# Kernel tuning notes

Hardware: AMD Instinct MI355X
Metric: run time of the kernel (lower is better)

Reference implementation:

```python
import jax, jax.numpy as jnp
import numpy as np

N_NODES = 50000
N_EDGES = 600000
FEAT = 128
N_RBF = 20
CUTOFF = 5.0


def setup_inputs() -> dict:
    key = jax.random.key(0)
    ks = jax.random.split(key, 8)
    s_j = jax.random.normal(ks[0], (N_NODES, FEAT), dtype=jnp.float32)
    # distances in (0.1, cutoff) to avoid div-by-zero in the sinc basis
    dist = jax.random.uniform(ks[1], (N_EDGES,), dtype=jnp.float32) * (CUTOFF - 0.1) + 0.1
    nbrs = jax.random.randint(ks[2], (N_EDGES, 2), 0, N_NODES, dtype=jnp.int64)
    scale = 1.0 / np.sqrt(FEAT)
    W1 = jax.random.normal(ks[3], (FEAT, FEAT), dtype=jnp.float32) * scale
    b1 = jnp.zeros((FEAT,), dtype=jnp.float32)
    W2 = jax.random.normal(ks[4], (FEAT, 3 * FEAT), dtype=jnp.float32) * scale
    b2 = jnp.zeros((3 * FEAT,), dtype=jnp.float32)
    Wd = jax.random.normal(ks[5], (N_RBF, 3 * FEAT), dtype=jnp.float32) / np.sqrt(N_RBF)
    bd = jnp.zeros((3 * FEAT,), dtype=jnp.float32)
    return {"s_j": s_j, "dist": dist, "nbrs": nbrs,
            "W1": W1, "b1": b1, "W2": W2, "b2": b2, "Wd": Wd, "bd": bd}


def _radial_basis(dist):
    # sin(n*pi*d/cutoff)/d for n = 1..N_RBF  -> [E, N_RBF]
    n = jnp.arange(1, N_RBF + 1, dtype=dist.dtype)
    d = dist[:, None]
    return jnp.sin(n * jnp.pi * d / CUTOFF) / d


def reference(s_j, dist, nbrs, W1, b1, W2, b2, Wd, bd):
    # gather neighbor features: [E, FEAT]
    sj = s_j[nbrs[:, 1]]
    # 2-layer MLP with swish: [E, 3*FEAT]
    h = sj @ W1 + b1
    h = h * jax.nn.sigmoid(h)  # swish
    phi = h @ W2 + b2
    # distance embedding: RBF -> dense: [E, 3*FEAT]
    w_s = _radial_basis(dist) @ Wd + bd
    out = phi * w_s
    return out.reshape(out.shape[0], -1, 3)  # [E, FEAT, 3]
```

## Files before the change

kernel.cpp:

```cpp
#include <hip/hip_runtime.h>
#include <math.h>

#define FEAT 128
#define OUTF 384
#define NRBF 20
#define EILP 8

typedef float f32x2 __attribute__((ext_vector_type(2)));
typedef float f32x4 __attribute__((ext_vector_type(4)));
typedef _Float16 f16x4 __attribute__((ext_vector_type(4)));
typedef _Float16 f16x8 __attribute__((ext_vector_type(8)));

__device__ __forceinline__ int nbrs_is_i64(const int* nb) {
    int nz = 0;
#pragma unroll
    for (int i = 1; i < 64; i += 2) nz |= nb[i];
    return nz == 0;
}

__global__ __launch_bounds__(256) void prep_w_kernel(
    const float* __restrict__ W1, const float* __restrict__ W2,
    _Float16* __restrict__ w1f, _Float16* __restrict__ w2f)
{
    int idx = blockIdx.x * 256 + threadIdx.x;
    if (idx < 8 * 4 * 64) {
        int ct = idx >> 8, ks = (idx >> 6) & 3, lane = idx & 63;
        int lcol = lane & 15, lgrp = lane >> 4;
        _Float16* dst = w1f + (size_t)idx * 8;
        const float* src = W1 + (size_t)(ks * 32 + lgrp * 8) * FEAT + ct * 16 + lcol;
#pragma unroll
        for (int j = 0; j < 8; j++) dst[j] = (_Float16)src[(size_t)j * FEAT];
    } else {
        int i2 = idx - 2048;
        if (i2 < 24 * 4 * 64) {
            int ct = i2 >> 8, ks = (i2 >> 6) & 3, lane = i2 & 63;
            int lcol = lane & 15, lgrp = lane >> 4;
            _Float16* dst = w2f + (size_t)i2 * 8;
            const float* src = W2 + (size_t)(ks * 32 + lgrp * 8) * OUTF + ct * 16 + lcol;
#pragma unroll
            for (int j = 0; j < 8; j++) dst[j] = (_Float16)src[(size_t)j * OUTF];
        }
    }
}

__global__ __launch_bounds__(256) void phi_mfma_kernel(
    const float* __restrict__ s_j,
    const _Float16* __restrict__ w1f, const float* __restrict__ b1,
    const _Float16* __restrict__ w2f, const float* __restrict__ b2,
    _Float16* __restrict__ PHI, int M)
{
    __shared__ __align__(16) float s32[64][136];
    __shared__ __align__(16) _Float16 h16[4][16][144];
    const int t = threadIdx.x;
    const int base = blockIdx.x * 64;

    for (int idx = t; idx < 64 * 32; idx += 256) {
        int row = idx >> 5, c4 = (idx & 31) * 4;
        float4 v = {0.f, 0.f, 0.f, 0.f};
        if (base + row < M) v = *(const float4*)(s_j + (size_t)(base + row) * FEAT + c4);
        *(float4*)&s32[row][c4] = v;
    }
    __syncthreads();

    const int w = t >> 6, lane = t & 63;
    const int lcol = lane & 15;
    const int lgrp = lane >> 4;
    const int r0 = w * 16;

    f16x8 a1[4];
#pragma unroll
    for (int ks = 0; ks < 4; ks++) {
        const float* p = &s32[r0 + lcol][ks * 32 + lgrp * 8];
        float4 u = *(const float4*)p;
        float4 v = *(const float4*)(p + 4);
        a1[ks] = (f16x8){(_Float16)u.x, (_Float16)u.y, (_Float16)u.z, (_Float16)u.w,
                         (_Float16)v.x, (_Float16)v.y, (_Float16)v.z, (_Float16)v.w};
    }

#pragma unroll
    for (int ct = 0; ct < 8; ct++) {
        float bb = b1[ct * 16 + lcol];
        f32x4 acc = {bb, bb, bb, bb};
#pragma unroll
        for (int ks = 0; ks < 4; ks++) {
            f16x8 b = *(const f16x8*)(w1f + ((size_t)(ct * 4 + ks) * 64 + lane) * 8);
            acc = __builtin_amdgcn_mfma_f32_16x16x32_f16(a1[ks], b, acc, 0, 0, 0);
        }
#pragma unroll
        for (int r = 0; r < 4; r++) {
            float h = acc[r];
            h = h * __frcp_rn(1.f + __expf(-h));
            h16[w][lgrp * 4 + r][ct * 16 + lcol] = (_Float16)h;
        }
    }

    f16x8 a2[4];
#pragma unroll
    for (int ks = 0; ks < 4; ks++)
        a2[ks] = *(const f16x8*)&h16[w][lcol][ks * 32 + lgrp * 8];

    for (int ch = 0; ch < 3; ch++) {
#pragma unroll
        for (int c8 = 0; c8 < 8; c8++) {
            int ct = ch * 8 + c8;
            float bb = b2[ct * 16 + lcol];
            f32x4 acc = {bb, bb, bb, bb};
#pragma unroll
            for (int ks = 0; ks < 4; ks++) {
                f16x8 b = *(const f16x8*)(w2f + ((size_t)(ct * 4 + ks) * 64 + lane) * 8);
                acc = __builtin_amdgcn_mfma_f32_16x16x32_f16(a2[ks], b, acc, 0, 0, 0);
            }
#pragma unroll
            for (int r = 0; r < 4; r++)
                h16[w][lgrp * 4 + r][c8 * 16 + lcol] = (_Float16)acc[r];
        }
#pragma unroll
        for (int i = 0; i < 4; i++) {
            int flat = i * 64 + lane;
            int row = flat >> 4, cc = (flat & 15) * 8;
            int grow = base + r0 + row;
            if (grow < M) {
                f16x8 v = *(const f16x8*)&h16[w][row][cc];
                *(f16x8*)(PHI + (size_t)grow * OUTF + ch * 128 + cc) = v;
            }
        }
    }
}

template <bool GATHER, bool HALF_OUT>
__global__ __launch_bounds__(256) void phi_kernel(
    const float* __restrict__ s_j, const int* __restrict__ nbrs,
    const float* __restrict__ W1, const float* __restrict__ b1,
    const float* __restrict__ W2, const float* __restrict__ b2,
    void* __restrict__ dst_v, int M)
{
    __shared__ __align__(16) float st[FEAT][66];
    const int t = threadIdx.x;
    const int base = blockIdx.x * 64;

    int i64f = 0;
    if (GATHER) i64f = nbrs_is_i64(nbrs);

    for (int idx = t; idx < 64 * FEAT; idx += 256) {
        int n = idx >> 7, k = idx & 127;
        int row = base + n;
        float v = 0.f;
        if (row < M) {
            int src = GATHER ? (i64f ? nbrs[4 * (size_t)row + 2] : nbrs[2 * (size_t)row + 1])
                             : row;
            v = s_j[(size_t)src * FEAT + k];
        }
        st[k][n] = v;
    }
    __syncthreads();

    const int cg = t & 31, rg = t >> 5;
    const int c0 = cg * 4, r0 = rg * 8;

    float acc[8][4];
    {
        float4 b = *(const float4*)(b1 + c0);
#pragma unroll
        for (int i = 0; i < 8; i++) { acc[i][0] = b.x; acc[i][1] = b.y; acc[i][2] = b.z; acc[i][3] = b.w; }
#pragma unroll 4
        for (int k = 0; k < FEAT; k++) {
            float4 w = *(const float4*)(W1 + (size_t)k * FEAT + c0);
            float2 sa = *(const float2*)(&st[k][r0]);
            float2 sb = *(const float2*)(&st[k][r0 + 2]);
            float2 sc = *(const float2*)(&st[k][r0 + 4]);
            float2 sd = *(const float2*)(&st[k][r0 + 6]);
            float sv[8] = {sa.x, sa.y, sb.x, sb.y, sc.x, sc.y, sd.x, sd.y};
#pragma unroll
            for (int i = 0; i < 8; i++) {
                acc[i][0] += sv[i] * w.x; acc[i][1] += sv[i] * w.y;
                acc[i][2] += sv[i] * w.z; acc[i][3] += sv[i] * w.w;
            }
        }
    }
    __syncthreads();
#pragma unroll
    for (int i = 0; i < 8; i++)
#pragma unroll
        for (int j = 0; j < 4; j++) {
            float h = acc[i][j];
            h = h * __frcp_rn(1.f + __expf(-h));
            st[c0 + j][r0 + i] = h;
        }
    __syncthreads();

    for (int ch = 0; ch < 3; ch++) {
        const int oc = ch * 128 + c0;
        float4 b = *(const float4*)(b2 + oc);
#pragma unroll
        for (int i = 0; i < 8; i++) { acc[i][0] = b.x; acc[i][1] = b.y; acc[i][2] = b.z; acc[i][3] = b.w; }
#pragma unroll 4
        for (int k = 0; k < FEAT; k++) {
            float4 w = *(const float4*)(W2 + (size_t)k * OUTF + oc);
            float2 ha = *(const float2*)(&st[k][r0]);
            float2 hb = *(const float2*)(&st[k][r0 + 2]);
            float2 hc = *(const float2*)(&st[k][r0 + 4]);
            float2 hd = *(const float2*)(&st[k][r0 + 6]);
            float hv[8] = {ha.x, ha.y, hb.x, hb.y, hc.x, hc.y, hd.x, hd.y};
#pragma unroll
            for (int i = 0; i < 8; i++) {
                acc[i][0] += hv[i] * w.x; acc[i][1] += hv[i] * w.y;
                acc[i][2] += hv[i] * w.z; acc[i][3] += hv[i] * w.w;
            }
        }
#pragma unroll
        for (int i = 0; i < 8; i++) {
            int row = base + r0 + i;
            if (row < M) {
                if (HALF_OUT) {
                    f16x4 o = {(_Float16)acc[i][0], (_Float16)acc[i][1],
                               (_Float16)acc[i][2], (_Float16)acc[i][3]};
                    *(f16x4*)((_Float16*)dst_v + (size_t)row * OUTF + oc) = o;
                } else {
                    float4 o = {acc[i][0], acc[i][1], acc[i][2], acc[i][3]};
                    *(float4*)((float*)dst_v + (size_t)row * OUTF + oc) = o;
                }
            }
        }
    }
}

template <bool FP16PHI>
__global__ __launch_bounds__(384)
__attribute__((amdgpu_waves_per_eu(3, 3)))
void edge_kernel(
    const float* __restrict__ dist, const int* __restrict__ nbrs,
    const void* phi_v, const float* __restrict__ Wd,
    const float* __restrict__ bd, float* out,
    int E, int gather)
{
    __shared__ __align__(16) f32x4 wdl[NRBF][96];
    const int t = threadIdx.x;
    for (int idx = t; idx < NRBF * 96; idx += 384) {
        int n = idx / 96, qq = idx % 96;
        wdl[n][qq] = *(const f32x4*)(Wd + (size_t)n * OUTF + qq * 4);
    }
    __syncthreads();

    const int g = t / 96;
    const int q = t % 96;
    const int c0 = q * 4;

    f32x4 bdr = *(const f32x4*)(bd + c0);

    int i64f = gather ? nbrs_is_i64(nbrs) : 0;
    const float kx = (float)(M_PI / 5.0);
    const int stride = gridDim.x * (4 * EILP);

    for (int e = (blockIdx.x * 4 + g) * EILP; e < E; e += stride) {
        float d[EILP];
        int r[EILP];
#pragma unroll
        for (int j = 0; j < EILP; j++) {
            int ej = e + j; if (ej >= E) ej = E - 1;
            d[j] = dist[ej];
            r[j] = gather ? (i64f ? nbrs[4 * (size_t)ej + 2] : nbrs[2 * (size_t)ej + 1]) : ej;
        }
        f32x4 p[EILP];
#pragma unroll
        for (int j = 0; j < EILP; j++) {
            if (FP16PHI) {
                const _Float16* ph = (const _Float16*)phi_v;
                f16x4 h = *(const f16x4*)(ph + (size_t)r[j] * OUTF + c0);
                p[j] = (f32x4){(float)h.x, (float)h.y, (float)h.z, (float)h.w};
            } else {
                const float* pf = (const float*)phi_v;
                p[j] = *(const f32x4*)(pf + (size_t)r[j] * OUTF + c0);
            }
        }

        float t2[EILP], sp[EILP], sc[EILP];
#pragma unroll
        for (int j = 0; j < EILP; j++) {
            float s, c;
            __sincosf(d[j] * kx, &s, &c);
            sc[j] = s;
            t2[j] = 2.f * c;
            sp[j] = 0.f;
        }
        f32x4 a[EILP];
#pragma unroll
        for (int j = 0; j < EILP; j++) a[j] = (f32x4){0.f, 0.f, 0.f, 0.f};
#pragma unroll
        for (int n = 0; n < NRBF; n++) {
            f32x4 w = wdl[n][q];
#pragma unroll
            for (int j = 0; j < EILP; j++) {
                a[j] += sc[j] * w;
                float nx = t2[j] * sc[j] - sp[j]; sp[j] = sc[j]; sc[j] = nx;
            }
        }
#pragma unroll
        for (int j = 0; j < EILP; j++) {
            if (e + j < E) {
                f32x4 o = p[j] * (a[j] * __frcp_rn(d[j]) + bdr);
                __builtin_nontemporal_store(o, (f32x4*)(out + (size_t)(e + j) * OUTF + c0));
            }
        }
    }
}

extern "C" void kernel_launch(void* const* d_in, const int* in_sizes, int n_in,
                              void* d_out, int out_size, void* d_ws, size_t ws_size,
                              hipStream_t stream)
{
    const float* s_j  = (const float*)d_in[0];
    const float* dist = (const float*)d_in[1];
    const int*   nbrs = (const int*)d_in[2];
    const float* W1   = (const float*)d_in[3];
    const float* b1   = (const float*)d_in[4];
    const float* W2   = (const float*)d_in[5];
    const float* b2   = (const float*)d_in[6];
    const float* Wd   = (const float*)d_in[7];
    const float* bd   = (const float*)d_in[8];
    float* out = (float*)d_out;

    const int N = in_sizes[0] / FEAT;
    const int E = in_sizes[1];
    if (E <= 0) return;

    const size_t phi_bytes = (size_t)N * OUTF * sizeof(_Float16);
    const size_t w1_off = phi_bytes;
    const size_t w2_off = w1_off + (size_t)8 * 4 * 64 * 8 * 2;
    const size_t need   = w2_off + (size_t)24 * 4 * 64 * 8 * 2;

    int egrid = (E + 4 * EILP - 1) / (4 * EILP);
    if (egrid > 2048) egrid = 2048;

    if (ws_size >= need) {
        _Float16* PHI = (_Float16*)d_ws;
        _Float16* w1f = (_Float16*)((char*)d_ws + w1_off);
        _Float16* w2f = (_Float16*)((char*)d_ws + w2_off);
        prep_w_kernel<<<32, 256, 0, stream>>>(W1, W2, w1f, w2f);
        phi_mfma_kernel<<<(N + 63) / 64, 256, 0, stream>>>(s_j, w1f, b1, w2f, b2, PHI, N);
        edge_kernel<true><<<egrid, 384, 0, stream>>>(dist, nbrs, PHI, Wd, bd, out, E, 1);
    } else {
        dim3 gA((E + 63) / 64);
        phi_kernel<true, false><<<gA, 256, 0, stream>>>(s_j, nbrs, W1, b1, W2, b2, d_out, E);
        edge_kernel<false><<<egrid, 384, 0, stream>>>(dist, nbrs, d_out, Wd, bd, out, E, 0);
    }
}
```

Measured before the change: 277.4 us.

## Compute distance embedding with fp16 MFMA in a new edge kernel

Adds an edge kernel that builds each edge's 20-term sinc radial basis in registers and multiplies it by a pre-packed fp16 Wd using a 16x16x32 MFMA, then scales by the gathered fp16 phi row. The prep kernel now also packs Wd into the MFMA operand layout. This removes the per-edge scalar FMA loop over RBF terms and the LDS staging of Wd. The trade-offs are fp16 rounding of the basis and weights, and output stores that are split into 64-byte pieces per edge row instead of contiguous full-row writes.

```diff
diff --git a/kernel.cpp b/kernel.cpp
--- a/kernel.cpp
+++ b/kernel.cpp
@@ -4,9 +4,7 @@
 #define FEAT 128
 #define OUTF 384
 #define NRBF 20
-#define EILP 8
-
-typedef float f32x2 __attribute__((ext_vector_type(2)));
+
 typedef float f32x4 __attribute__((ext_vector_type(4)));
 typedef _Float16 f16x4 __attribute__((ext_vector_type(4)));
 typedef _Float16 f16x8 __attribute__((ext_vector_type(8)));
@@ -20,7 +18,9 @@
 
 __global__ __launch_bounds__(256) void prep_w_kernel(
     const float* __restrict__ W1, const float* __restrict__ W2,
-    _Float16* __restrict__ w1f, _Float16* __restrict__ w2f)
+    const float* __restrict__ Wd,
+    _Float16* __restrict__ w1f, _Float16* __restrict__ w2f,
+    _Float16* __restrict__ wdf)
 {
     int idx = blockIdx.x * 256 + threadIdx.x;
     if (idx < 8 * 4 * 64) {
@@ -30,15 +30,26 @@
         const float* src = W1 + (size_t)(ks * 32 + lgrp * 8) * FEAT + ct * 16 + lcol;
 #pragma unroll
         for (int j = 0; j < 8; j++) dst[j] = (_Float16)src[(size_t)j * FEAT];
+    } else if (idx < 8192) {
+        int i2 = idx - 2048;
+        int ct = i2 >> 8, ks = (i2 >> 6) & 3, lane = i2 & 63;
+        int lcol = lane & 15, lgrp = lane >> 4;
+        _Float16* dst = w2f + (size_t)i2 * 8;
+        const float* src = W2 + (size_t)(ks * 32 + lgrp * 8) * OUTF + ct * 16 + lcol;
+#pragma unroll
+        for (int j = 0; j < 8; j++) dst[j] = (_Float16)src[(size_t)j * OUTF];
     } else {
-        int i2 = idx - 2048;
-        if (i2 < 24 * 4 * 64) {
-            int ct = i2 >> 8, ks = (i2 >> 6) & 3, lane = i2 & 63;
+        int i3 = idx - 8192;
+        if (i3 < 24 * 64) {
+            int ct = i3 >> 6, lane = i3 & 63;
             int lcol = lane & 15, lgrp = lane >> 4;
-            _Float16* dst = w2f + (size_t)i2 * 8;
-            const float* src = W2 + (size_t)(ks * 32 + lgrp * 8) * OUTF + ct * 16 + lcol;
-#pragma unroll
-            for (int j = 0; j < 8; j++) dst[j] = (_Float16)src[(size_t)j * OUTF];
+            _Float16* dst = wdf + (size_t)i3 * 8;
+#pragma unroll
+            for (int j = 0; j < 8; j++) {
+                int k = lgrp * 8 + j;
+                dst[j] = (k < NRBF) ? (_Float16)Wd[(size_t)k * OUTF + ct * 16 + lcol]
+                                    : (_Float16)0.f;
+            }
         }
     }
 }
@@ -127,12 +138,74 @@
     }
 }
 
-template <bool GATHER, bool HALF_OUT>
+__global__ __launch_bounds__(256) void edge_mfma_kernel(
+    const float* __restrict__ dist, const int* __restrict__ nbrs,
+    const _Float16* __restrict__ PHI, const _Float16* __restrict__ wdf,
+    const float* __restrict__ bd, float* __restrict__ out, int E)
+{
+    const int t = threadIdx.x;
+    const int w = t >> 6, lane = t & 63;
+    const int lcol = lane & 15, lgrp = lane >> 4;
+
+    const int i64f = nbrs_is_i64(nbrs);
+    const int e = blockIdx.x * 64 + w * 16 + lcol;
+    const int ec = (e < E) ? e : (E - 1);
+    const bool ok = (e < E);
+
+    const float d = dist[ec];
+    const int ridx = i64f ? nbrs[4 * (size_t)ec + 2] : nbrs[2 * (size_t)ec + 1];
+
+    const float kx = (float)(M_PI / 5.0);
+    float v[NRBF];
+    {
+        float s, c;
+        __sincosf(d * kx, &s, &c);
+        float rd = __frcp_rn(d);
+        float t2 = 2.f * c;
+        float sp = 0.f, sc = s;
+        v[0] = s * rd;
+#pragma unroll
+        for (int n = 1; n < NRBF; n++) {
+            float nx = t2 * sc - sp; sp = sc; sc = nx;
+            v[n] = sc * rd;
+        }
+    }
+    f16x8 bf;
+    if (lgrp == 0)
+        bf = (f16x8){(_Float16)v[0], (_Float16)v[1], (_Float16)v[2], (_Float16)v[3],
+                     (_Float16)v[4], (_Float16)v[5], (_Float16)v[6], (_Float16)v[7]};
+    else if (lgrp == 1)
+        bf = (f16x8){(_Float16)v[8], (_Float16)v[9], (_Float16)v[10], (_Float16)v[11],
+                     (_Float16)v[12], (_Float16)v[13], (_Float16)v[14], (_Float16)v[15]};
+    else if (lgrp == 2)
+        bf = (f16x8){(_Float16)v[16], (_Float16)v[17], (_Float16)v[18], (_Float16)v[19],
+                     (_Float16)0.f, (_Float16)0.f, (_Float16)0.f, (_Float16)0.f};
+    else
+        bf = (f16x8){(_Float16)0.f, (_Float16)0.f, (_Float16)0.f, (_Float16)0.f,
+                     (_Float16)0.f, (_Float16)0.f, (_Float16)0.f, (_Float16)0.f};
+
+    const _Float16* phirow = PHI + (size_t)ridx * OUTF;
+    float* orow = out + (size_t)ec * OUTF;
+
+#pragma unroll 4
+    for (int ct = 0; ct < 24; ct++) {
+        const int c0 = ct * 16 + lgrp * 4;
+        f16x8 af = *(const f16x8*)(wdf + ((size_t)(ct * 64 + lane)) * 8);
+        f32x4 acc = *(const f32x4*)(bd + c0);
+        acc = __builtin_amdgcn_mfma_f32_16x16x32_f16(af, bf, acc, 0, 0, 0);
+        f16x4 p = *(const f16x4*)(phirow + c0);
+        f32x4 o = {(float)p.x * acc[0], (float)p.y * acc[1],
+                   (float)p.z * acc[2], (float)p.w * acc[3]};
+        if (ok) __builtin_nontemporal_store(o, (f32x4*)(orow + c0));
+    }
+}
+
+template <bool GATHER>
 __global__ __launch_bounds__(256) void phi_kernel(
     const float* __restrict__ s_j, const int* __restrict__ nbrs,
     const float* __restrict__ W1, const float* __restrict__ b1,
     const float* __restrict__ W2, const float* __restrict__ b2,
-    void* __restrict__ dst_v, int M)
+    float* __restrict__ dst, int M)
 {
     __shared__ __align__(16) float st[FEAT][66];
     const int t = threadIdx.x;
@@ -211,27 +284,19 @@
         for (int i = 0; i < 8; i++) {
             int row = base + r0 + i;
             if (row < M) {
-                if (HALF_OUT) {
-                    f16x4 o = {(_Float16)acc[i][0], (_Float16)acc[i][1],
-                               (_Float16)acc[i][2], (_Float16)acc[i][3]};
-                    *(f16x4*)((_Float16*)dst_v + (size_t)row * OUTF + oc) = o;
-                } else {
-                    float4 o = {acc[i][0], acc[i][1], acc[i][2], acc[i][3]};
-                    *(float4*)((float*)dst_v + (size_t)row * OUTF + oc) = o;
-                }
-            }
-        }
-    }
-}
-
-template <bool FP16PHI>
+                float4 o = {acc[i][0], acc[i][1], acc[i][2], acc[i][3]};
+                *(float4*)(dst + (size_t)row * OUTF + oc) = o;
+            }
+        }
+    }
+}
+
 __global__ __launch_bounds__(384)
 __attribute__((amdgpu_waves_per_eu(3, 3)))
 void edge_kernel(
     const float* __restrict__ dist, const int* __restrict__ nbrs,
-    const void* phi_v, const float* __restrict__ Wd,
-    const float* __restrict__ bd, float* out,
-    int E, int gather)
+    const float* phi, const float* __restrict__ Wd,
+    const float* __restrict__ bd, float* out, int E)
 {
     __shared__ __align__(16) f32x4 wdl[NRBF][96];
     const int t = threadIdx.x;
@@ -244,58 +309,45 @@
     const int g = t / 96;
     const int q = t % 96;
     const int c0 = q * 4;
-
     f32x4 bdr = *(const f32x4*)(bd + c0);
 
-    int i64f = gather ? nbrs_is_i64(nbrs) : 0;
     const float kx = (float)(M_PI / 5.0);
-    const int stride = gridDim.x * (4 * EILP);
-
-    for (int e = (blockIdx.x * 4 + g) * EILP; e < E; e += stride) {
-        float d[EILP];
-        int r[EILP];
-#pragma unroll
-        for (int j = 0; j < EILP; j++) {
+    const int stride = gridDim.x * 32;
+
+    for (int e = (blockIdx.x * 4 + g) * 8; e < E; e += stride) {
+        float d[8]; int r[8];
+#pragma unroll
+        for (int j = 0; j < 8; j++) {
             int ej = e + j; if (ej >= E) ej = E - 1;
             d[j] = dist[ej];
-            r[j] = gather ? (i64f ? nbrs[4 * (size_t)ej + 2] : nbrs[2 * (size_t)ej + 1]) : ej;
-        }
-        f32x4 p[EILP];
-#pragma unroll
-        for (int j = 0; j < EILP; j++) {
-            if (FP16PHI) {
-                const _Float16* ph = (const _Float16*)phi_v;
-                f16x4 h = *(const f16x4*)(ph + (size_t)r[j] * OUTF + c0);
-                p[j] = (f32x4){(float)h.x, (float)h.y, (float)h.z, (float)h.w};
-            } else {
-                const float* pf = (const float*)phi_v;
-                p[j] = *(const f32x4*)(pf + (size_t)r[j] * OUTF + c0);
-            }
-        }
-
-        float t2[EILP], sp[EILP], sc[EILP];
-#pragma unroll
-        for (int j = 0; j < EILP; j++) {
+            r[j] = ej;
+        }
+        f32x4 p[8];
+#pragma unroll
+        for (int j = 0; j < 8; j++)
+            p[j] = *(const f32x4*)(phi + (size_t)r[j] * OUTF + c0);
+
+        float t2[8], sp[8], sc[8];
+#pragma unroll
+        for (int j = 0; j < 8; j++) {
             float s, c;
             __sincosf(d[j] * kx, &s, &c);
-            sc[j] = s;
-            t2[j] = 2.f * c;
-            sp[j] = 0.f;
-        }
-        f32x4 a[EILP];
-#pragma unroll
-        for (int j = 0; j < EILP; j++) a[j] = (f32x4){0.f, 0.f, 0.f, 0.f};
+            sc[j] = s; t2[j] = 2.f * c; sp[j] = 0.f;
+        }
+        f32x4 a[8];
+#pragma unroll
+        for (int j = 0; j < 8; j++) a[j] = (f32x4){0.f, 0.f, 0.f, 0.f};
 #pragma unroll
         for (int n = 0; n < NRBF; n++) {
-            f32x4 w = wdl[n][q];
-#pragma unroll
-            for (int j = 0; j < EILP; j++) {
-                a[j] += sc[j] * w;
+            f32x4 wv = wdl[n][q];
+#pragma unroll
+            for (int j = 0; j < 8; j++) {
+                a[j] += sc[j] * wv;
                 float nx = t2[j] * sc[j] - sp[j]; sp[j] = sc[j]; sc[j] = nx;
             }
         }
 #pragma unroll
-        for (int j = 0; j < EILP; j++) {
+        for (int j = 0; j < 8; j++) {
             if (e + j < E) {
                 f32x4 o = p[j] * (a[j] * __frcp_rn(d[j]) + bdr);
                 __builtin_nontemporal_store(o, (f32x4*)(out + (size_t)(e + j) * OUTF + c0));
@@ -324,23 +376,24 @@
     if (E <= 0) return;
 
     const size_t phi_bytes = (size_t)N * OUTF * sizeof(_Float16);
-    const size_t w1_off = phi_bytes;
-    const size_t w2_off = w1_off + (size_t)8 * 4 * 64 * 8 * 2;
-    const size_t need   = w2_off + (size_t)24 * 4 * 64 * 8 * 2;
-
-    int egrid = (E + 4 * EILP - 1) / (4 * EILP);
-    if (egrid > 2048) egrid = 2048;
+    const size_t w1_off  = phi_bytes;
+    const size_t w2_off  = w1_off + (size_t)8 * 4 * 64 * 8 * 2;
+    const size_t wdf_off = w2_off + (size_t)24 * 4 * 64 * 8 * 2;
+    const size_t need    = wdf_off + (size_t)24 * 64 * 8 * 2;
 
     if (ws_size >= need) {
         _Float16* PHI = (_Float16*)d_ws;
         _Float16* w1f = (_Float16*)((char*)d_ws + w1_off);
         _Float16* w2f = (_Float16*)((char*)d_ws + w2_off);
-        prep_w_kernel<<<32, 256, 0, stream>>>(W1, W2, w1f, w2f);
+        _Float16* wdf = (_Float16*)((char*)d_ws + wdf_off);
+        prep_w_kernel<<<38, 256, 0, stream>>>(W1, W2, Wd, w1f, w2f, wdf);
         phi_mfma_kernel<<<(N + 63) / 64, 256, 0, stream>>>(s_j, w1f, b1, w2f, b2, PHI, N);
-        edge_kernel<true><<<egrid, 384, 0, stream>>>(dist, nbrs, PHI, Wd, bd, out, E, 1);
+        edge_mfma_kernel<<<(E + 63) / 64, 256, 0, stream>>>(dist, nbrs, PHI, wdf, bd, out, E);
     } else {
         dim3 gA((E + 63) / 64);
-        phi_kernel<true, false><<<gA, 256, 0, stream>>>(s_j, nbrs, W1, b1, W2, b2, d_out, E);
-        edge_kernel<false><<<egrid, 384, 0, stream>>>(dist, nbrs, d_out, Wd, bd, out, E, 0);
-    }
-}
+        phi_kernel<true><<<gA, 256, 0, stream>>>(s_j, nbrs, W1, b1, W2, b2, out, E);
+        int egrid = (E + 31) / 32;
+        if (egrid > 2048) egrid = 2048;
+        edge_kernel<<<egrid, 384, 0, stream>>>(dist, nbrs, out, Wd, bd, out, E);
+    }
+}
```

New measurement: 308.2 us. 11.1% more time.
